# Optimization experiments

Measured on AMD Instinct MI355X. Metric: run time of the kernel, lower is better.

Reference implementation:

```python
import jax, jax.numpy as jnp
import numpy as np

B, S, H, NH, HD, I = 2, 1024, 4096, 32, 128, 11008
EPS = 1e-6
THETA = 10000.0


def _rmsnorm(x, w):
    v = jnp.mean(x * x, axis=-1, keepdims=True)
    return x * jax.lax.rsqrt(v + EPS) * w


def _quant(x):
    # per-tensor symmetric int8 quantization (scale already folded upstream)
    return jnp.clip(jnp.round(x), -128.0, 127.0)


def _lin_i8(xq_i8, w_i8, scale, bias):
    acc = jnp.matmul(xq_i8.astype(jnp.int32), w_i8.astype(jnp.int32).T)
    return acc.astype(jnp.float32) * scale + bias


def _rope(q, k):
    pos = jnp.arange(S, dtype=jnp.float32)
    inv = 1.0 / (THETA ** (jnp.arange(0, HD, 2, dtype=jnp.float32) / HD))
    f = pos[:, None] * inv[None, :]              # [S, HD/2]
    emb = jnp.concatenate([f, f], axis=-1)        # [S, HD]
    cos = jnp.cos(emb)[None, None]                # [1,1,S,HD]
    sin = jnp.sin(emb)[None, None]
    def rot(x):
        return jnp.concatenate([-x[..., HD // 2:], x[..., :HD // 2]], axis=-1)
    return q * cos + rot(q) * sin, k * cos + rot(k) * sin


def setup_inputs() -> dict:
    key = jax.random.key(0)
    ks = jax.random.split(key, 30)
    def w8(k, o, i):
        return jax.random.randint(k, (o, i), -128, 128, dtype=jnp.int8)
    def sc(k):
        return jax.random.uniform(k, (), jnp.float32, 0.001, 0.01)
    return {
        "hidden_states": jax.random.normal(ks[0], (B, S, H), jnp.float32),
        "ln1_w": jax.random.uniform(ks[1], (H,), jnp.float32, 0.5, 1.5) * 20.0,
        "ln2_w": jax.random.uniform(ks[2], (H,), jnp.float32, 0.5, 1.5) * 20.0,
        "Wq": w8(ks[3], H, H), "Wk": w8(ks[4], H, H), "Wv": w8(ks[5], H, H),
        "Wo": w8(ks[6], H, H),
        "Wg": w8(ks[7], I, H), "Wu": w8(ks[8], I, H), "Wd": w8(ks[9], H, I),
        "bq": jax.random.normal(ks[10], (H,), jnp.float32) * 0.01,
        "bk": jax.random.normal(ks[11], (H,), jnp.float32) * 0.01,
        "bv": jax.random.normal(ks[12], (H,), jnp.float32) * 0.01,
        "bo": jax.random.normal(ks[13], (H,), jnp.float32) * 0.01,
        "bg": jax.random.normal(ks[14], (I,), jnp.float32) * 0.01,
        "bu": jax.random.normal(ks[15], (I,), jnp.float32) * 0.01,
        "bd": jax.random.normal(ks[16], (H,), jnp.float32) * 0.01,
        "sq": sc(ks[17]) * 1e-3, "sk": sc(ks[18]) * 1e-3, "sv": sc(ks[19]) * 1e-3,
        "so": sc(ks[20]) * 1e-3, "sg": sc(ks[21]) * 1e-3, "su": sc(ks[22]) * 1e-3,
        "sd": sc(ks[23]) * 1e-3,
        "o_in_scale": sc(ks[24]), "down_in_scale": sc(ks[25]),
    }


def reference(hidden_states, ln1_w, ln2_w, Wq, Wk, Wv, Wo, Wg, Wu, Wd,
              bq, bk, bv, bo, bg, bu, bd,
              sq, sk, sv, so, sg, su, sd, o_in_scale, down_in_scale):
    residual = hidden_states
    # input RMSNorm (quant scale folded into ln1_w) -> int8 activation
    hq = _quant(_rmsnorm(hidden_states, ln1_w)).astype(jnp.int8)
    q = _lin_i8(hq, Wq, sq, bq).reshape(B, S, NH, HD).transpose(0, 2, 1, 3)
    k = _lin_i8(hq, Wk, sk, bk).reshape(B, S, NH, HD).transpose(0, 2, 1, 3)
    v = _lin_i8(hq, Wv, sv, bv).reshape(B, S, NH, HD).transpose(0, 2, 1, 3)
    q, k = _rope(q, k)
    scores = jnp.einsum("bhqd,bhkd->bhqk", q, k) / np.float32(np.sqrt(HD))
    causal = jnp.tril(jnp.ones((S, S), dtype=bool))
    scores = jnp.where(causal[None, None], scores, jnp.float32(-1e30))
    attn = jax.nn.softmax(scores, axis=-1)
    o = jnp.einsum("bhqk,bhkd->bhqd", attn, v).transpose(0, 2, 1, 3).reshape(B, S, H)
    # o_proj with quant scale (W8A8BFP32OFP32LinearWithQuantScale)
    oq = _quant(o / o_in_scale).astype(jnp.int8)
    h = residual + _lin_i8(oq, Wo, so, bo)
    residual = h
    # post-attention RMSNorm (fc1 quant scale folded into ln2_w)
    hq2 = _quant(_rmsnorm(h, ln2_w)).astype(jnp.int8)
    g = _lin_i8(hq2, Wg, sg, bg)
    u = _lin_i8(hq2, Wu, su, bu)
    a = jax.nn.silu(g) * u
    aq = _quant(a / down_in_scale).astype(jnp.int8)
    out = residual + _lin_i8(aq, Wd, sd, bd)
    return out
```

## Files before the change

kernel.cpp:

```cpp
#include <hip/hip_runtime.h>
#include <math.h>

#define B_  2
#define S_  1024
#define H_  4096
#define NH_ 32
#define HD_ 128
#define I_  11008
#define R_  2048

typedef __attribute__((ext_vector_type(4))) int i32x4;
typedef __attribute__((ext_vector_type(4))) float f32x4;
typedef __attribute__((ext_vector_type(8))) short bf16x8;


__device__ __forceinline__ void gload_lds16(const void* g, void* l) {
    __builtin_amdgcn_global_load_lds(
        (const __attribute__((address_space(1))) unsigned int*)g,
        (__attribute__((address_space(3))) unsigned int*)l, 16, 0, 0);
}

__device__ __forceinline__ unsigned short f2bf(float f) {
    unsigned int u = __float_as_uint(f);
    u += 0x7fffu + ((u >> 16) & 1u);
    return (unsigned short)(u >> 16);
}

__global__ __launch_bounds__(256)
void packW_k(const int* __restrict__ W, signed char* __restrict__ out, const int K)
{
    const int kt = blockIdx.x, cb = blockIdx.y, nk = gridDim.x;
    const int t = threadIdx.x;
    int* otile = (int*)(out + ((long)(cb * nk + kt) << 13));
#pragma unroll
    for (int i = 0; i < 8; ++i) {
        const int o = i * 256 + t;
        const int g = o >> 9, r = (o >> 2) & 127, jj = o & 3;
        const int4 w4 = *(const int4*)(W + (long)(cb * 128 + r) * K + kt * 64 + g * 16 + jj * 4);
        otile[o] = (w4.x & 255) | ((w4.y & 255) << 8) | ((w4.z & 255) << 16) | (w4.w << 24);
    }
}

__global__ __launch_bounds__(256)
void rmsnorm_quant_k(const float* __restrict__ x, const float* __restrict__ w,
                     signed char* __restrict__ out)
{
    __shared__ float red[4];
    const int tid = threadIdx.x;
    const long row = blockIdx.x;
    const float4* xr = (const float4*)(x + row * H_);
    float4 xv[4];
    float ss = 0.f;
#pragma unroll
    for (int i = 0; i < 4; ++i) {
        xv[i] = xr[tid + i * 256];
        ss += xv[i].x * xv[i].x + xv[i].y * xv[i].y
            + xv[i].z * xv[i].z + xv[i].w * xv[i].w;
    }
#pragma unroll
    for (int off = 32; off; off >>= 1) ss += __shfl_xor(ss, off);
    if ((tid & 63) == 0) red[tid >> 6] = ss;
    __syncthreads();
    const float tot = red[0] + red[1] + red[2] + red[3];
    const float sc = 1.f / sqrtf(tot * (1.f / (float)H_) + 1e-6f);
    const float4* wr = (const float4*)w;
    int* ob = (int*)out;
    const long rb = row >> 7;
    const int rr = (int)(row & 127);
#pragma unroll
    for (int i = 0; i < 4; ++i) {
        const float4 wv = wr[tid + i * 256];
        const int b0 = (int)fminf(fmaxf(rintf(xv[i].x * sc * wv.x), -128.f), 127.f);
        const int b1 = (int)fminf(fmaxf(rintf(xv[i].y * sc * wv.y), -128.f), 127.f);
        const int b2 = (int)fminf(fmaxf(rintf(xv[i].z * sc * wv.z), -128.f), 127.f);
        const int b3 = (int)fminf(fmaxf(rintf(xv[i].w * sc * wv.w), -128.f), 127.f);
        const int packed = (b0 & 255) | ((b1 & 255) << 8) | ((b2 & 255) << 16) | (b3 << 24);
        const int j4 = tid + i * 256;
        const long a32 = ((rb * 64 + (j4 >> 4)) << 11) + (((j4 >> 2) & 3) << 9)
                       + (rr << 2) + (j4 & 3);
        ob[a32] = packed;
    }
}

template<int MODE>
__global__ __launch_bounds__(256, 3)
void gemm_i8t(const signed char* __restrict__ A8, const signed char* __restrict__ W8,
              const float* __restrict__ scale_ptr, const float* __restrict__ bias,
              const float* __restrict__ residual, float* __restrict__ C,
              const float* __restrict__ gbuf, const float* __restrict__ qscale,
              signed char* __restrict__ out8,
              const int N, const int K, const int gx)
{
    __shared__ __align__(16) signed char lsA[3][8192];
    __shared__ __align__(16) signed char lsB[3][8192];

    int bid = blockIdx.x;
    {
        const int nwg = gridDim.x;
        const int q = nwg >> 3, r = nwg & 7;
        const int xcd = bid & 7, idx = bid >> 3;
        bid = (xcd < r) ? (xcd * (q + 1) + idx)
                        : (r * (q + 1) + (xcd - r) * q + idx);
    }
    const int bx = bid % gx, by = bid / gx;

    const int tid  = threadIdx.x;
    const int lane = tid & 63, wid = tid >> 6;
    const int bm = bx << 7, bn = by << 7;
    const int wm = (wid >> 1) << 6, wn = (wid & 1) << 6;

    i32x4 acc[4][4];
#pragma unroll
    for (int m = 0; m < 4; ++m)
#pragma unroll
        for (int n = 0; n < 4; ++n) acc[m][n] = (i32x4){0, 0, 0, 0};

    const int nk = K >> 6;
    const signed char* abase = A8 + ((long)bx * nk << 13);
    const signed char* bbase = W8 + ((long)by * nk << 13);
    const int so0 = wid * 2048 + lane * 16;
    const int ld0 = wid * 2048;

#pragma unroll
    for (int t = 0; t < 2; ++t) {
        const signed char* at = abase + ((long)t << 13);
        const signed char* bt = bbase + ((long)t << 13);
        gload_lds16(at + so0,        lsA[t] + ld0);
        gload_lds16(at + so0 + 1024, lsA[t] + ld0 + 1024);
        gload_lds16(bt + so0,        lsB[t] + ld0);
        gload_lds16(bt + so0 + 1024, lsB[t] + ld0 + 1024);
    }

    for (int kt = 0; kt < nk; ++kt) {
        const int cur = kt % 3;
        if (kt + 2 < nk) {
            const int pb = (kt + 2) % 3;
            const signed char* at = abase + ((long)(kt + 2) << 13);
            const signed char* bt = bbase + ((long)(kt + 2) << 13);
            gload_lds16(at + so0,        lsA[pb] + ld0);
            gload_lds16(at + so0 + 1024, lsA[pb] + ld0 + 1024);
            gload_lds16(bt + so0,        lsB[pb] + ld0);
            gload_lds16(bt + so0 + 1024, lsB[pb] + ld0 + 1024);
        }
        if (kt + 2 < nk)      asm volatile("s_waitcnt vmcnt(8)" ::: "memory");
        else if (kt + 1 < nk) asm volatile("s_waitcnt vmcnt(4)" ::: "memory");
        else                  asm volatile("s_waitcnt vmcnt(0)" ::: "memory");
        __builtin_amdgcn_s_barrier();

        const int kg = (lane >> 4) * 2048, fr = (lane & 15) * 16;
        i32x4 af[4], bf[4];
#pragma unroll
        for (int m = 0; m < 4; ++m)
            af[m] = *(const i32x4*)(lsA[cur] + kg + wm * 16 + m * 256 + fr);
#pragma unroll
        for (int n = 0; n < 4; ++n)
            bf[n] = *(const i32x4*)(lsB[cur] + kg + wn * 16 + n * 256 + fr);
        __builtin_amdgcn_s_setprio(1);
#pragma unroll
        for (int m = 0; m < 4; ++m)
#pragma unroll
            for (int n = 0; n < 4; ++n)
                acc[m][n] = __builtin_amdgcn_mfma_i32_16x16x64_i8(af[m], bf[n], acc[m][n], 0, 0, 0);
        __builtin_amdgcn_s_setprio(0);
        __builtin_amdgcn_s_barrier();
    }

    const float s = *scale_ptr;
    const int rq = (lane >> 4) * 4, fc = lane & 15;
    if (MODE == 0) {
#pragma unroll
        for (int m = 0; m < 4; ++m) {
#pragma unroll
            for (int n = 0; n < 4; ++n) {
                const int col = bn + wn + n * 16 + fc;
                const float bcol = bias[col];
#pragma unroll
                for (int r = 0; r < 4; ++r) {
                    const int row = bm + wm + m * 16 + rq + r;
                    float v = (float)acc[m][n][r] * s + bcol;
                    if (residual) v += residual[(long)row * N + col];
                    C[(long)row * N + col] = v;
                }
            }
        }
    } else {
        const float dinv = 1.f / qscale[0];
        const int nko = N >> 6;
#pragma unroll
        for (int m = 0; m < 4; ++m) {
#pragma unroll
            for (int n = 0; n < 4; ++n) {
                const int col = bn + wn + n * 16 + fc;
                const float bcol = bias[col];
                const int ktc = col >> 6, kgc = (col >> 4) & 3, jc = col & 15;
#pragma unroll
                for (int r = 0; r < 4; ++r) {
                    const int row = bm + wm + m * 16 + rq + r;
                    const float u = (float)acc[m][n][r] * s + bcol;
                    const float g = gbuf[(long)row * N + col];
                    const float a = g / (1.f + __expf(-g)) * u;
                    const float qv = fminf(fmaxf(rintf(a * dinv), -128.f), 127.f);
                    const long addr = (((long)(row >> 7) * nko + ktc) << 13)
                                    + (kgc << 11) + ((row & 127) << 4) + jc;
                    out8[addr] = (signed char)(int)qv;
                }
            }
        }
    }
}

__global__ __launch_bounds__(256)
void rope_k(float* __restrict__ q, float* __restrict__ k)
{
    const int row = blockIdx.x;
    const int s = row & (S_ - 1);
    float* qr = q + (long)row * H_;
    float* kr = k + (long)row * H_;
    for (int t = threadIdx.x; t < NH_ * 64; t += 256) {
        const int nh = t >> 6, i = t & 63;
        const float inv = powf(10000.f, -(float)(2 * i) * (1.f / 128.f));
        const float f = (float)s * inv;
        float sn, c;
        sincosf(f, &sn, &c);
        const int base = nh * 128 + i;
        const float q0 = qr[base], q1 = qr[base + 64];
        qr[base]      = q0 * c - q1 * sn;
        qr[base + 64] = q1 * c + q0 * sn;
        const float k0 = kr[base], k1 = kr[base + 64];
        kr[base]      = k0 * c - k1 * sn;
        kr[base + 64] = k1 * c + k0 * sn;
    }
}

__global__ __launch_bounds__(256, 2)
void attn_mfma_k(const float* __restrict__ q, const float* __restrict__ k,
                 const float* __restrict__ v, signed char* __restrict__ out8,
                 const float* __restrict__ osc)
{
    __shared__ __align__(16) char lsK[8192];
    __shared__ __align__(16) char lsV[10240];
    __shared__ __align__(16) char lsP[4][1024];

    const int tid = threadIdx.x, lane = tid & 63, wid = tid >> 6;
    const int bid = blockIdx.x;
    const int qt = 15 - (bid >> 6);
    const int bh = bid & 63;
    const int b = bh >> 5, h = bh & 31;
    const int q0 = qt * 64;
    const int qw = q0 + wid * 16;

    const float* qbase = q + (long)(b * S_) * H_ + (long)h * HD_;
    const float* kbase = k + (long)(b * S_) * H_ + (long)h * HD_;
    const float* vbase = v + (long)(b * S_) * H_ + (long)h * HD_;

    const int frow = lane & 15, fgrp = lane >> 4;
    const float sc = 0.08838834764831845f;

    bf16x8 qf[4];
    {
        const float* qr = qbase + (long)(qw + frow) * H_;
#pragma unroll
        for (int c = 0; c < 4; ++c) {
            const float4 a = *(const float4*)(qr + c * 32 + fgrp * 8);
            const float4 bq = *(const float4*)(qr + c * 32 + fgrp * 8 + 4);
            bf16x8 t;
            t[0] = (short)f2bf(a.x * sc);  t[1] = (short)f2bf(a.y * sc);
            t[2] = (short)f2bf(a.z * sc);  t[3] = (short)f2bf(a.w * sc);
            t[4] = (short)f2bf(bq.x * sc); t[5] = (short)f2bf(bq.y * sc);
            t[6] = (short)f2bf(bq.z * sc); t[7] = (short)f2bf(bq.w * sc);
            qf[c] = t;
        }
    }

    f32x4 oacc[8];
#pragma unroll
    for (int n2 = 0; n2 < 8; ++n2) oacc[n2] = (f32x4){0.f, 0.f, 0.f, 0.f};
    float mr[4] = {-1e30f, -1e30f, -1e30f, -1e30f};
    float lr[4] = {0.f, 0.f, 0.f, 0.f};

    const int nt = (q0 >> 5) + 2;
    for (int kt = 0; kt < nt; ++kt) {
        if (kt) __syncthreads();
        {
            const float* kg = kbase + (long)(kt * 32) * H_;
            const float* vg = vbase + (long)(kt * 32) * H_;
#pragma unroll
            for (int i = 0; i < 4; ++i) {
                const int lin = i * 256 + tid;
                const int kr = lin >> 5;
                const int d4 = (lin & 31) * 4;
                const float4 kv = *(const float4*)(kg + (long)kr * H_ + d4);
                const float4 vv = *(const float4*)(vg + (long)kr * H_ + d4);
                ushort4 kb;
                kb.x = f2bf(kv.x); kb.y = f2bf(kv.y); kb.z = f2bf(kv.z); kb.w = f2bf(kv.w);
                *(ushort4*)(lsK + kr * 256 + ((d4 * 2) ^ ((kr & 7) << 4))) = kb;
                *(unsigned short*)(lsV + (d4 + 0) * 80 + kr * 2) = f2bf(vv.x);
                *(unsigned short*)(lsV + (d4 + 1) * 80 + kr * 2) = f2bf(vv.y);
                *(unsigned short*)(lsV + (d4 + 2) * 80 + kr * 2) = f2bf(vv.z);
                *(unsigned short*)(lsV + (d4 + 3) * 80 + kr * 2) = f2bf(vv.w);
            }
        }
        __syncthreads();

        if (kt * 32 <= qw + 15) {
            f32x4 s0 = (f32x4){0.f, 0.f, 0.f, 0.f};
            f32x4 s1 = (f32x4){0.f, 0.f, 0.f, 0.f};
            const int swz = (frow & 7) << 4;
#pragma unroll
            for (int c = 0; c < 4; ++c) {
                const int dby = c * 64 + fgrp * 16;
                const bf16x8 kfA = *(const bf16x8*)(lsK + frow * 256 + (dby ^ swz));
                const bf16x8 kfB = *(const bf16x8*)(lsK + (frow + 16) * 256 + (dby ^ swz));
                s0 = __builtin_amdgcn_mfma_f32_16x16x32_bf16(qf[c], kfA, s0, 0, 0, 0);
                s1 = __builtin_amdgcn_mfma_f32_16x16x32_bf16(qf[c], kfB, s1, 0, 0, 0);
            }

            const int colg0 = kt * 32 + frow;
            float cf[4];
#pragma unroll
            for (int r = 0; r < 4; ++r) {
                const int rowg = qw + fgrp * 4 + r;
                const float a0 = (colg0 <= rowg) ? s0[r] : -1e30f;
                const float a1 = (colg0 + 16 <= rowg) ? s1[r] : -1e30f;
                float mx = fmaxf(a0, a1);
#pragma unroll
                for (int off2 = 1; off2 < 16; off2 <<= 1) mx = fmaxf(mx, __shfl_xor(mx, off2));
                const float mnew = fmaxf(mr[r], mx);
                cf[r] = __expf(mr[r] - mnew);
                mr[r] = mnew;
                const float p0 = __expf(a0 - mnew);
                const float p1 = __expf(a1 - mnew);
                float sm = p0 + p1;
#pragma unroll
                for (int off2 = 1; off2 < 16; off2 <<= 1) sm += __shfl_xor(sm, off2);
                lr[r] = lr[r] * cf[r] + sm;
                const int row = fgrp * 4 + r;
                const int psw = (row & 3) << 4;
                *(unsigned short*)(lsP[wid] + row * 64 + ((frow * 2) ^ psw)) = f2bf(p0);
                *(unsigned short*)(lsP[wid] + row * 64 + (((16 + frow) * 2) ^ psw)) = f2bf(p1);
            }
#pragma unroll
            for (int n2 = 0; n2 < 8; ++n2) {
#pragma unroll
                for (int r = 0; r < 4; ++r) oacc[n2][r] *= cf[r];
            }
            const bf16x8 pf = *(const bf16x8*)(lsP[wid] + frow * 64 + ((fgrp * 16) ^ ((frow & 3) << 4)));
#pragma unroll
            for (int n2 = 0; n2 < 8; ++n2) {
                const bf16x8 vf = *(const bf16x8*)(lsV + (n2 * 16 + frow) * 80 + fgrp * 16);
                oacc[n2] = __builtin_amdgcn_mfma_f32_16x16x32_bf16(pf, vf, oacc[n2], 0, 0, 0);
            }
        }
    }

    const float oinv = 1.f / osc[0];
    float inv[4];
#pragma unroll
    for (int r = 0; r < 4; ++r) inv[r] = 1.f / lr[r];
#pragma unroll
    for (int n2 = 0; n2 < 8; ++n2) {
        const int kk = h * 128 + n2 * 16 + frow;
        const int ktc = kk >> 6, kgc = (kk >> 4) & 3, jc = kk & 15;
#pragma unroll
        for (int r = 0; r < 4; ++r) {
            const int rowt = b * S_ + qw + fgrp * 4 + r;
            const float ov = oacc[n2][r] * inv[r];
            const float qv = fminf(fmaxf(rintf(ov * oinv), -128.f), 127.f);
            const long addr = (((long)(rowt >> 7) * 64 + ktc) << 13)
                            + (kgc << 11) + ((rowt & 127) << 4) + jc;
            out8[addr] = (signed char)(int)qv;
        }
    }
}

extern "C" void kernel_launch(void* const* d_in, const int* in_sizes, int n_in,
                              void* d_out, int out_size, void* d_ws, size_t ws_size,
                              hipStream_t stream)
{
    const float* hidden = (const float*)d_in[0];
    const float* ln1 = (const float*)d_in[1];
    const float* ln2 = (const float*)d_in[2];
    const int* Wq = (const int*)d_in[3];
    const int* Wk = (const int*)d_in[4];
    const int* Wv = (const int*)d_in[5];
    const int* Wo = (const int*)d_in[6];
    const int* Wg = (const int*)d_in[7];
    const int* Wu = (const int*)d_in[8];
    const int* Wd = (const int*)d_in[9];
    const float* bq = (const float*)d_in[10];
    const float* bk = (const float*)d_in[11];
    const float* bv = (const float*)d_in[12];
    const float* bo = (const float*)d_in[13];
    const float* bg = (const float*)d_in[14];
    const float* bu = (const float*)d_in[15];
    const float* bd = (const float*)d_in[16];
    const float* sq = (const float*)d_in[17];
    const float* sk = (const float*)d_in[18];
    const float* sv = (const float*)d_in[19];
    const float* so = (const float*)d_in[20];
    const float* sg = (const float*)d_in[21];
    const float* su = (const float*)d_in[22];
    const float* sd = (const float*)d_in[23];
    const float* o_sc = (const float*)d_in[24];
    const float* d_sc = (const float*)d_in[25];

    char* ws = (char*)d_ws;
    signed char* HQ8 = (signed char*)ws;
    signed char* WP  = (signed char*)(ws + ((size_t)22 << 20));
    float* Qb = (float*)(ws + ((size_t)66 << 20));
    float* Kb = (float*)(ws + ((size_t)98 << 20));
    float* Vb = (float*)(ws + ((size_t)130 << 20));
    float* Gb = (float*)(ws + ((size_t)98 << 20));
    signed char* AQ8 = (signed char*)(ws + ((size_t)184 << 20));
    float* Hb = Qb;
    float* out = (float*)d_out;

    const dim3 blk(256);
    const int gxH = R_ / 128;
    const int nwgH = gxH * (H_ / 128);
    const int nwgI = gxH * (I_ / 128);
    const dim3 gpH(H_ / 64, H_ / 128);
    const dim3 gpI(H_ / 64, I_ / 128);
    const dim3 gpD(I_ / 64, H_ / 128);

    rmsnorm_quant_k<<<R_, blk, 0, stream>>>(hidden, ln1, HQ8);

    packW_k<<<gpH, blk, 0, stream>>>(Wq, WP, H_);
    gemm_i8t<0><<<nwgH, blk, 0, stream>>>(HQ8, WP, sq, bq, nullptr, Qb,
                                          nullptr, nullptr, nullptr, H_, H_, gxH);
    packW_k<<<gpH, blk, 0, stream>>>(Wk, WP, H_);
    gemm_i8t<0><<<nwgH, blk, 0, stream>>>(HQ8, WP, sk, bk, nullptr, Kb,
                                          nullptr, nullptr, nullptr, H_, H_, gxH);
    packW_k<<<gpH, blk, 0, stream>>>(Wv, WP, H_);
    gemm_i8t<0><<<nwgH, blk, 0, stream>>>(HQ8, WP, sv, bv, nullptr, Vb,
                                          nullptr, nullptr, nullptr, H_, H_, gxH);

    rope_k<<<R_, blk, 0, stream>>>(Qb, Kb);
    attn_mfma_k<<<B_ * NH_ * (S_ / 64), blk, 0, stream>>>(Qb, Kb, Vb, HQ8, o_sc);

    packW_k<<<gpH, blk, 0, stream>>>(Wo, WP, H_);
    gemm_i8t<0><<<nwgH, blk, 0, stream>>>(HQ8, WP, so, bo, hidden, Hb,
                                          nullptr, nullptr, nullptr, H_, H_, gxH);

    rmsnorm_quant_k<<<R_, blk, 0, stream>>>(Hb, ln2, HQ8);

    packW_k<<<gpI, blk, 0, stream>>>(Wg, WP, H_);
    gemm_i8t<0><<<nwgI, blk, 0, stream>>>(HQ8, WP, sg, bg, nullptr, Gb,
                                          nullptr, nullptr, nullptr, I_, H_, gxH);
    packW_k<<<gpI, blk, 0, stream>>>(Wu, WP, H_);
    gemm_i8t<1><<<nwgI, blk, 0, stream>>>(HQ8, WP, su, bu, nullptr, nullptr,
                                          Gb, d_sc, AQ8, I_, H_, gxH);
    packW_k<<<gpD, blk, 0, stream>>>(Wd, WP, I_);
    gemm_i8t<0><<<nwgH, blk, 0, stream>>>(AQ8, WP, sd, bd, Hb, out,
                                          nullptr, nullptr, nullptr, H_, I_, gxH);
}
```

Baseline: 997.1 us.

## Switch int8 GEMM to double-buffered 128-wide K tiles

```diff
diff --git a/kernel.cpp b/kernel.cpp
--- a/kernel.cpp
+++ b/kernel.cpp
@@ -83,7 +83,7 @@
 }
 
 template<int MODE>
-__global__ __launch_bounds__(256, 3)
+__global__ __launch_bounds__(256, 2)
 void gemm_i8t(const signed char* __restrict__ A8, const signed char* __restrict__ W8,
               const float* __restrict__ scale_ptr, const float* __restrict__ bias,
               const float* __restrict__ residual, float* __restrict__ C,
@@ -91,8 +91,8 @@
               signed char* __restrict__ out8,
               const int N, const int K, const int gx)
 {
-    __shared__ __align__(16) signed char lsA[3][8192];
-    __shared__ __align__(16) signed char lsB[3][8192];
+    __shared__ __align__(16) signed char lsA[2][16384];
+    __shared__ __align__(16) signed char lsB[2][16384];
 
     int bid = blockIdx.x;
     {
@@ -115,53 +115,54 @@
 #pragma unroll
         for (int n = 0; n < 4; ++n) acc[m][n] = (i32x4){0, 0, 0, 0};
 
-    const int nk = K >> 6;
+    const int nk  = K >> 6;
+    const int nk2 = K >> 7;
     const signed char* abase = A8 + ((long)bx * nk << 13);
     const signed char* bbase = W8 + ((long)by * nk << 13);
-    const int so0 = wid * 2048 + lane * 16;
-    const int ld0 = wid * 2048;
-
-#pragma unroll
-    for (int t = 0; t < 2; ++t) {
-        const signed char* at = abase + ((long)t << 13);
-        const signed char* bt = bbase + ((long)t << 13);
-        gload_lds16(at + so0,        lsA[t] + ld0);
-        gload_lds16(at + so0 + 1024, lsA[t] + ld0 + 1024);
-        gload_lds16(bt + so0,        lsB[t] + ld0);
-        gload_lds16(bt + so0 + 1024, lsB[t] + ld0 + 1024);
-    }
-
-    for (int kt = 0; kt < nk; ++kt) {
-        const int cur = kt % 3;
-        if (kt + 2 < nk) {
-            const int pb = (kt + 2) % 3;
-            const signed char* at = abase + ((long)(kt + 2) << 13);
-            const signed char* bt = bbase + ((long)(kt + 2) << 13);
-            gload_lds16(at + so0,        lsA[pb] + ld0);
-            gload_lds16(at + so0 + 1024, lsA[pb] + ld0 + 1024);
-            gload_lds16(bt + so0,        lsB[pb] + ld0);
-            gload_lds16(bt + so0 + 1024, lsB[pb] + ld0 + 1024);
-        }
-        if (kt + 2 < nk)      asm volatile("s_waitcnt vmcnt(8)" ::: "memory");
-        else if (kt + 1 < nk) asm volatile("s_waitcnt vmcnt(4)" ::: "memory");
-        else                  asm volatile("s_waitcnt vmcnt(0)" ::: "memory");
+    const int sgg = wid * 4096 + lane * 16;
+    const int sgl = wid * 4096;
+
+#pragma unroll
+    for (int c = 0; c < 4; ++c) {
+        gload_lds16(abase + sgg + c * 1024, lsA[0] + sgl + c * 1024);
+        gload_lds16(bbase + sgg + c * 1024, lsB[0] + sgl + c * 1024);
+    }
+
+    for (int kt = 0; kt < nk2; ++kt) {
+        const int cur = kt & 1, nxt = cur ^ 1;
+        if (kt + 1 < nk2) {
+            const signed char* at = abase + ((long)(kt + 1) << 14);
+            const signed char* bt = bbase + ((long)(kt + 1) << 14);
+#pragma unroll
+            for (int c = 0; c < 4; ++c) {
+                gload_lds16(at + sgg + c * 1024, lsA[nxt] + sgl + c * 1024);
+                gload_lds16(bt + sgg + c * 1024, lsB[nxt] + sgl + c * 1024);
+            }
+            asm volatile("s_waitcnt vmcnt(8)" ::: "memory");
+        } else {
+            asm volatile("s_waitcnt vmcnt(0)" ::: "memory");
+        }
         __builtin_amdgcn_s_barrier();
 
         const int kg = (lane >> 4) * 2048, fr = (lane & 15) * 16;
-        i32x4 af[4], bf[4];
-#pragma unroll
-        for (int m = 0; m < 4; ++m)
-            af[m] = *(const i32x4*)(lsA[cur] + kg + wm * 16 + m * 256 + fr);
-#pragma unroll
-        for (int n = 0; n < 4; ++n)
-            bf[n] = *(const i32x4*)(lsB[cur] + kg + wn * 16 + n * 256 + fr);
-        __builtin_amdgcn_s_setprio(1);
-#pragma unroll
-        for (int m = 0; m < 4; ++m)
+#pragma unroll
+        for (int s = 0; s < 2; ++s) {
+            const int off = s * 8192;
+            i32x4 af[4], bf[4];
+#pragma unroll
+            for (int m = 0; m < 4; ++m)
+                af[m] = *(const i32x4*)(lsA[cur] + off + kg + wm * 16 + m * 256 + fr);
 #pragma unroll
             for (int n = 0; n < 4; ++n)
-                acc[m][n] = __builtin_amdgcn_mfma_i32_16x16x64_i8(af[m], bf[n], acc[m][n], 0, 0, 0);
-        __builtin_amdgcn_s_setprio(0);
+                bf[n] = *(const i32x4*)(lsB[cur] + off + kg + wn * 16 + n * 256 + fr);
+            __builtin_amdgcn_s_setprio(1);
+#pragma unroll
+            for (int m = 0; m < 4; ++m)
+#pragma unroll
+                for (int n = 0; n < 4; ++n)
+                    acc[m][n] = __builtin_amdgcn_mfma_i32_16x16x64_i8(af[m], bf[n], acc[m][n], 0, 0, 0);
+            __builtin_amdgcn_s_setprio(0);
+        }
         __builtin_amdgcn_s_barrier();
     }
 
```

Result: faster. 941.4 us (-5.6%).
